# Kernel optimization log

Measured on AMD Instinct MI355X. Metric: run time of the kernel, lower is better.

## Reference

```python
import jax, jax.numpy as jnp
import numpy as np

B, S, D, H = 2, 2048, 1024, 16
HD = D // H  # head_dim = 64


def setup_inputs() -> dict:
    key = jax.random.key(0)
    ks = jax.random.split(key, 11)
    sc = 0.02
    inp = {
        "q": jax.random.normal(ks[0], (B, S, D), jnp.float32),
        "k": jax.random.normal(ks[1], (B, S, D), jnp.float32),
        "v": jax.random.normal(ks[2], (B, S, D), jnp.float32),
        # causal mask, broadcast over batch and heads; mask==0 positions get -1e9
        "mask": jnp.tril(jnp.ones((S, S), dtype=bool))[None, None, :, :],
        "Wq": jax.random.normal(ks[3], (D, D), jnp.float32) * sc,
        "bq": jnp.zeros((D,), jnp.float32),
        "Wk": jax.random.normal(ks[4], (D, D), jnp.float32) * sc,
        "bk": jnp.zeros((D,), jnp.float32),
        "Wv": jax.random.normal(ks[5], (D, D), jnp.float32) * sc,
        "bv": jnp.zeros((D,), jnp.float32),
        "Wo": jax.random.normal(ks[6], (D, D), jnp.float32) * sc,
        "bo": jnp.zeros((D,), jnp.float32),
    }
    return inp


def reference(q, k, v, Wq, bq, Wk, bk, Wv, bv, Wo, bo, mask):
    b, s, d = q.shape
    scale = 1.0 / jnp.sqrt(jnp.asarray(HD, q.dtype))

    def proj(x, W, bias):
        # nn.Linear: x @ W.T + b ; then split heads -> [b, h, s, hd]
        return (x @ W.T + bias).reshape(b, -1, H, HD).transpose(0, 2, 1, 3)

    Qh = proj(q, Wq, bq)
    Kh = proj(k, Wk, bk)
    Vh = proj(v, Wv, bv)

    scores = jnp.einsum("bhqd,bhkd->bhqk", Qh, Kh) * scale
    scores = jnp.where(mask, scores, jnp.asarray(-1e9, scores.dtype))
    probs = jax.nn.softmax(scores, axis=-1)
    attn = jnp.einsum("bhqk,bhkd->bhqd", probs, Vh)
    attn = attn.transpose(0, 2, 1, 3).reshape(b, -1, d)
    return attn @ Wo.T + bo
```

## Files before the change

### kernel.cpp

```cpp
#include <hip/hip_runtime.h>
#include <math.h>

#define B_ 2
#define S_ 2048
#define D_ 1024
#define H_ 16
#define HD_ 64

typedef __bf16 bf16;
typedef bf16 bf16x8_t __attribute__((ext_vector_type(8)));
typedef short s16x8 __attribute__((ext_vector_type(8)));
typedef float f32x4 __attribute__((ext_vector_type(4)));

static __device__ __forceinline__ f32x4 mfma16(s16x8 a, s16x8 b, f32x4 c) {
  return __builtin_amdgcn_mfma_f32_16x16x32_bf16(a, b, c, 0, 0, 0);
}

static __device__ __forceinline__ s16x8 cvt2x4(f32x4 a, f32x4 b) {
  bf16x8_t t;
  t[0] = (bf16)a[0]; t[1] = (bf16)a[1]; t[2] = (bf16)a[2]; t[3] = (bf16)a[3];
  t[4] = (bf16)b[0]; t[5] = (bf16)b[1]; t[6] = (bf16)b[2]; t[7] = (bf16)b[3];
  return __builtin_bit_cast(s16x8, t);
}

static __device__ __forceinline__ void gl16(const bf16* g, bf16* l) {
  __builtin_amdgcn_global_load_lds((const __attribute__((address_space(1))) void*)g,
                                   (__attribute__((address_space(3))) void*)l, 16, 0, 0);
}

__global__ __launch_bounds__(256) void cvt_w(
    const float* __restrict__ Wq, const float* __restrict__ Wk,
    const float* __restrict__ Wv, bf16* __restrict__ dst) {
  const float* s = blockIdx.y == 0 ? Wq : (blockIdx.y == 1 ? Wk : Wv);
  bf16* d = dst + (size_t)blockIdx.y * D_ * D_;
  const int i = (blockIdx.x * 256 + threadIdx.x) * 8;
  f32x4 a = *(const f32x4*)(s + i);
  f32x4 b = *(const f32x4*)(s + i + 4);
  *(s16x8*)(d + i) = cvt2x4(a, b);
}

__global__ __launch_bounds__(256) void cvt_w1(
    const float* __restrict__ W, bf16* __restrict__ dst) {
  const int i = (blockIdx.x * 256 + threadIdx.x) * 8;
  f32x4 a = *(const f32x4*)(W + i);
  f32x4 b = *(const f32x4*)(W + i + 4);
  *(s16x8*)(dst + i) = cvt2x4(a, b);
}

__global__ __launch_bounds__(256) void qkv_gemm(
    const float* __restrict__ q, const float* __restrict__ k, const float* __restrict__ v,
    const bf16* __restrict__ Wb,
    const float* __restrict__ bq, const float* __restrict__ bk, const float* __restrict__ bv,
    bf16* __restrict__ Qh, bf16* __restrict__ Kh, bf16* __restrict__ Vt) {
  __shared__ bf16 lA[128][72];
  __shared__ bf16 lB[128][64];
  const int tid = threadIdx.x, lane = tid & 63, wave = tid >> 6;
  const int wsel = blockIdx.y >> 3;
  const int col0 = (blockIdx.y & 7) * 128;
  const int row0 = blockIdx.x * 128;
  const float* X = wsel == 0 ? q : (wsel == 1 ? k : v);
  const bf16* W = Wb + (size_t)wsel * D_ * D_;
  const float* bias = wsel == 0 ? bq : (wsel == 1 ? bk : bv);

  const int lr = lane & 15, g = lane >> 4, lk = g * 8;
  const int wrow = (wave >> 1) * 64, wcol = (wave & 1) * 64;

  const int arow = tid >> 1, aseg = (tid & 1) * 32;
  const float* Xp = X + (size_t)(row0 + arow) * D_ + aseg;

  const bf16* Wp = W + (size_t)(col0 + wave * 32 + (lane >> 3)) * D_ +
                   (size_t)(((lane & 7) ^ ((lane >> 3) & 7)) * 8);
  bf16* lBw = &lB[wave * 32][0];

  f32x4 acc[4][4] = {};
  f32x4 xr[8];
#pragma unroll
  for (int j = 0; j < 8; j++) xr[j] = *(const f32x4*)(Xp + j * 4);

  for (int kk = 0; kk < D_; kk += 64) {
    __syncthreads();
#pragma unroll
    for (int p = 0; p < 4; p++)
      *(s16x8*)&lA[arow][aseg + p * 8] = cvt2x4(xr[2 * p], xr[2 * p + 1]);
#pragma unroll
    for (int i = 0; i < 4; i++)
      gl16(Wp + (size_t)i * 8 * D_ + kk, lBw + i * 8 * 64);
    __syncthreads();
    if (kk + 64 < D_) {
#pragma unroll
      for (int j = 0; j < 8; j++) xr[j] = *(const f32x4*)(Xp + kk + 64 + j * 4);
    }

    s16x8 af[4][2], bfr[4][2];
#pragma unroll
    for (int mi = 0; mi < 4; mi++)
#pragma unroll
      for (int kd = 0; kd < 2; kd++)
        af[mi][kd] = *(const s16x8*)&lA[wrow + mi * 16 + lr][kd * 32 + lk];
#pragma unroll
    for (int ni = 0; ni < 4; ni++)
#pragma unroll
      for (int kd = 0; kd < 2; kd++)
        bfr[ni][kd] = *(const s16x8*)((const bf16*)lB +
                        (size_t)(wcol + ni * 16 + lr) * 64 +
                        (((4 * kd + g) ^ (lr & 7)) * 8));
    __builtin_amdgcn_s_setprio(1);
#pragma unroll
    for (int mi = 0; mi < 4; mi++)
#pragma unroll
      for (int ni = 0; ni < 4; ni++)
#pragma unroll
        for (int kd = 0; kd < 2; kd++)
          acc[mi][ni] = mfma16(af[mi][kd], bfr[ni][kd], acc[mi][ni]);
    __builtin_amdgcn_s_setprio(0);
  }

  const int rb = g * 4;
#pragma unroll
  for (int mi = 0; mi < 4; mi++) {
#pragma unroll
    for (int ni = 0; ni < 4; ni++) {
      const int col = col0 + wcol + ni * 16 + lr;
      const int h = col >> 6, hd = col & 63;
      const float bvv = bias[col];
#pragma unroll
      for (int r = 0; r < 4; r++) {
        const int row = row0 + wrow + mi * 16 + rb + r;
        const int b = row >> 11, s = row & (S_ - 1);
        const float val = acc[mi][ni][r] + bvv;
        if (wsel == 0)
          Qh[(((size_t)(b * H_ + h)) * S_ + s) * HD_ + hd] = (bf16)(val * 0.125f);
        else if (wsel == 1)
          Kh[(((size_t)(b * H_ + h)) * S_ + s) * HD_ + hd] = (bf16)val;
        else
          Vt[(((size_t)(b * H_ + h)) * HD_ + hd) * S_ + s] = (bf16)val;
      }
    }
  }
}

__global__ __launch_bounds__(256) void out_gemm(
    const bf16* __restrict__ X, const bf16* __restrict__ W,
    const float* __restrict__ bias, float* __restrict__ Y) {
  __shared__ bf16 lA[64][64];
  __shared__ bf16 lB[128][64];
  const int tid = threadIdx.x, lane = tid & 63, wave = tid >> 6;
  const int row0 = blockIdx.x * 64, col0 = blockIdx.y * 128;
  const int lr = lane & 15, g = lane >> 4, lk = g * 8;
  const int wrow = (wave >> 1) * 32, wcol = (wave & 1) * 64;
  const int csw = ((lane & 7) ^ ((lane >> 3) & 7)) * 8;

  const bf16* Ap = X + (size_t)(row0 + wave * 16 + (lane >> 3)) * D_ + csw;
  const bf16* Wp = W + (size_t)(col0 + wave * 32 + (lane >> 3)) * D_ + csw;
  bf16* lAw = &lA[wave * 16][0];
  bf16* lBw = &lB[wave * 32][0];

  f32x4 acc[2][4] = {};
  for (int kk = 0; kk < D_; kk += 64) {
    __syncthreads();
#pragma unroll
    for (int i = 0; i < 2; i++) gl16(Ap + (size_t)i * 8 * D_ + kk, lAw + i * 8 * 64);
#pragma unroll
    for (int i = 0; i < 4; i++) gl16(Wp + (size_t)i * 8 * D_ + kk, lBw + i * 8 * 64);
    __syncthreads();

    s16x8 af[2][2], bfr[4][2];
#pragma unroll
    for (int mi = 0; mi < 2; mi++)
#pragma unroll
      for (int kd = 0; kd < 2; kd++)
        af[mi][kd] = *(const s16x8*)((const bf16*)lA +
                       (size_t)(wrow + mi * 16 + lr) * 64 +
                       (((4 * kd + g) ^ (lr & 7)) * 8));
#pragma unroll
    for (int ni = 0; ni < 4; ni++)
#pragma unroll
      for (int kd = 0; kd < 2; kd++)
        bfr[ni][kd] = *(const s16x8*)((const bf16*)lB +
                        (size_t)(wcol + ni * 16 + lr) * 64 +
                        (((4 * kd + g) ^ (lr & 7)) * 8));
    __builtin_amdgcn_s_setprio(1);
#pragma unroll
    for (int mi = 0; mi < 2; mi++)
#pragma unroll
      for (int ni = 0; ni < 4; ni++)
#pragma unroll
        for (int kd = 0; kd < 2; kd++)
          acc[mi][ni] = mfma16(af[mi][kd], bfr[ni][kd], acc[mi][ni]);
    __builtin_amdgcn_s_setprio(0);
  }

  const int rb = g * 4;
#pragma unroll
  for (int mi = 0; mi < 2; mi++) {
#pragma unroll
    for (int ni = 0; ni < 4; ni++) {
      const int col = col0 + wcol + ni * 16 + lr;
      const float bvv = bias[col];
#pragma unroll
      for (int r = 0; r < 4; r++) {
        const int row = row0 + wrow + mi * 16 + rb + r;
        Y[(size_t)row * D_ + col] = acc[mi][ni][r] + bvv;
      }
    }
  }
}

__global__ __launch_bounds__(256) void attn_fwd(
    const bf16* __restrict__ Qh, const bf16* __restrict__ Kh,
    const bf16* __restrict__ Vt, bf16* __restrict__ attnO) {
  __shared__ bf16 k_lds[64][72];
  __shared__ bf16 vt_lds[64][72];
  __shared__ bf16 p_lds[4][32][72];
  __shared__ float red_lds[4][32];

  const int tid = threadIdx.x;
  const int lane = tid & 63, wave = tid >> 6;
  const int lr = lane & 15, g = lane >> 4, lk = g * 8, rb = g * 4;

  const int bidx = blockIdx.x;
  const int qb = 15 - (bidx >> 5);
  const int bh = bidx & 31;
  const int bb = bh >> 4, hh = bh & 15;
  const int q0w = qb * 128 + wave * 32;

  const bf16* Q = Qh + (size_t)bh * S_ * HD_;
  const bf16* K = Kh + (size_t)bh * S_ * HD_;
  const bf16* Vp = Vt + (size_t)bh * HD_ * S_;

  s16x8 qf[2][2];
#pragma unroll
  for (int qfi = 0; qfi < 2; qfi++)
#pragma unroll
    for (int kd = 0; kd < 2; kd++)
      qf[qfi][kd] = *(const s16x8*)(Q + (size_t)(q0w + qfi * 16 + lr) * HD_ + kd * 32 + lk);

  f32x4 o[2][4] = {};
  float m_run[2] = {-INFINITY, -INFINITY};
  float l_run[2] = {0.0f, 0.0f};

  const int srow = tid >> 2, d0 = (tid & 3) << 4;
  const int ntiles = qb * 2 + 2;

  s16x8 kr0, kr1, vr0, vr1;
  {
    const bf16* kp = K + (size_t)srow * HD_ + d0;
    kr0 = *(const s16x8*)kp;
    kr1 = *(const s16x8*)(kp + 8);
    const bf16* vp = Vp + (size_t)srow * S_ + d0;
    vr0 = *(const s16x8*)vp;
    vr1 = *(const s16x8*)(vp + 8);
  }

  for (int t = 0; t < ntiles; t++) {
    const int k0 = t * 64;
    __syncthreads();
    *(s16x8*)&k_lds[srow][d0] = kr0;
    *(s16x8*)&k_lds[srow][d0 + 8] = kr1;
    *(s16x8*)&vt_lds[srow][d0] = vr0;
    *(s16x8*)&vt_lds[srow][d0 + 8] = vr1;
    __syncthreads();
    if (t + 1 < ntiles) {
      const int kn = k0 + 64;
      const bf16* kp = K + (size_t)(kn + srow) * HD_ + d0;
      kr0 = *(const s16x8*)kp;
      kr1 = *(const s16x8*)(kp + 8);
      const bf16* vp = Vp + (size_t)srow * S_ + kn + d0;
      vr0 = *(const s16x8*)vp;
      vr1 = *(const s16x8*)(vp + 8);
    }

    if (k0 <= q0w + 31) {
      const bool doMask = (k0 + 63 > q0w);
      s16x8 kfr[4][2];
#pragma unroll
      for (int kf = 0; kf < 4; kf++)
#pragma unroll
        for (int kd = 0; kd < 2; kd++)
          kfr[kf][kd] = *(const s16x8*)&k_lds[kf * 16 + lr][kd * 32 + lk];
      f32x4 s[4][2];
#pragma unroll
      for (int kf = 0; kf < 4; kf++)
#pragma unroll
        for (int qfi = 0; qfi < 2; qfi++) s[kf][qfi] = (f32x4){0.f, 0.f, 0.f, 0.f};
      __builtin_amdgcn_s_setprio(1);
#pragma unroll
      for (int kf = 0; kf < 4; kf++)
#pragma unroll
        for (int qfi = 0; qfi < 2; qfi++)
#pragma unroll
          for (int kd = 0; kd < 2; kd++)
            s[kf][qfi] = mfma16(kfr[kf][kd], qf[qfi][kd], s[kf][qfi]);
      __builtin_amdgcn_s_setprio(0);

#pragma unroll
      for (int qfi = 0; qfi < 2; qfi++) {
        const int qg = q0w + qfi * 16 + lr;
        if (doMask) {
#pragma unroll
          for (int kf = 0; kf < 4; kf++)
#pragma unroll
            for (int r = 0; r < 4; r++)
              if (k0 + kf * 16 + rb + r > qg) s[kf][qfi][r] = -INFINITY;
        }
        float mx = fmaxf(fmaxf(s[0][qfi][0], s[0][qfi][1]), fmaxf(s[0][qfi][2], s[0][qfi][3]));
#pragma unroll
        for (int kf = 1; kf < 4; kf++)
          mx = fmaxf(mx, fmaxf(fmaxf(s[kf][qfi][0], s[kf][qfi][1]),
                               fmaxf(s[kf][qfi][2], s[kf][qfi][3])));
        mx = fmaxf(mx, __shfl_xor(mx, 16));
        mx = fmaxf(mx, __shfl_xor(mx, 32));
        const float mo = m_run[qfi];
        const float mn = fmaxf(mo, mx);
        const float corr = exp2f((mo - mn) * 1.44269504f);
        float ps = 0.0f;
#pragma unroll
        for (int kf = 0; kf < 4; kf++)
#pragma unroll
          for (int r = 0; r < 4; r++) {
            const float p = exp2f((s[kf][qfi][r] - mn) * 1.44269504f);
            s[kf][qfi][r] = p;
            ps += p;
          }
        ps += __shfl_xor(ps, 16);
        ps += __shfl_xor(ps, 32);
        l_run[qfi] = l_run[qfi] * corr + ps;
        m_run[qfi] = mn;
        if (g == 0) red_lds[wave][qfi * 16 + lr] = corr;
#pragma unroll
        for (int kf = 0; kf < 4; kf++)
#pragma unroll
          for (int rp = 0; rp < 2; rp++) {
            unsigned int lo = (unsigned int)__builtin_bit_cast(
                unsigned short, (bf16)s[kf][qfi][2 * rp]);
            unsigned int hi = (unsigned int)__builtin_bit_cast(
                unsigned short, (bf16)s[kf][qfi][2 * rp + 1]);
            *(unsigned int*)&p_lds[wave][qfi * 16 + lr][kf * 16 + rb + 2 * rp] =
                lo | (hi << 16);
          }
      }
#pragma unroll
      for (int rf = 0; rf < 2; rf++) {
        f32x4 c4 = *(const f32x4*)&red_lds[wave][rf * 16 + rb];
#pragma unroll
        for (int df = 0; df < 4; df++)
#pragma unroll
          for (int r = 0; r < 4; r++) o[rf][df][r] *= c4[r];
      }
      s16x8 vfr[4][2];
#pragma unroll
      for (int df = 0; df < 4; df++)
#pragma unroll
        for (int kk = 0; kk < 2; kk++)
          vfr[df][kk] = *(const s16x8*)&vt_lds[df * 16 + lr][kk * 32 + lk];
      __builtin_amdgcn_s_setprio(1);
#pragma unroll
      for (int rf = 0; rf < 2; rf++) {
        s16x8 pa[2];
#pragma unroll
        for (int kk = 0; kk < 2; kk++)
          pa[kk] = *(const s16x8*)&p_lds[wave][rf * 16 + lr][kk * 32 + lk];
#pragma unroll
        for (int df = 0; df < 4; df++)
#pragma unroll
          for (int kk = 0; kk < 2; kk++)
            o[rf][df] = mfma16(pa[kk], vfr[df][kk], o[rf][df]);
      }
      __builtin_amdgcn_s_setprio(0);
    }
  }

  if (g == 0) {
    red_lds[wave][lr] = l_run[0];
    red_lds[wave][16 + lr] = l_run[1];
  }
#pragma unroll
  for (int rf = 0; rf < 2; rf++) {
    f32x4 l4 = *(const f32x4*)&red_lds[wave][rf * 16 + rb];
    float inv[4];
#pragma unroll
    for (int r = 0; r < 4; r++) inv[r] = 1.0f / l4[r];
#pragma unroll
    for (int df = 0; df < 4; df++)
#pragma unroll
      for (int r = 0; r < 4; r++) {
        const int srw = q0w + rf * 16 + rb + r;
        const int dcol = df * 16 + lr;
        attnO[((size_t)(bb * S_ + srw)) * D_ + hh * HD_ + dcol] =
            (bf16)(o[rf][df][r] * inv[r]);
      }
  }
}

extern "C" void kernel_launch(void* const* d_in, const int* in_sizes, int n_in,
                              void* d_out, int out_size, void* d_ws, size_t ws_size,
                              hipStream_t stream) {
  const float* q  = (const float*)d_in[0];
  const float* k  = (const float*)d_in[1];
  const float* v  = (const float*)d_in[2];
  const float* Wq = (const float*)d_in[4];
  const float* bq = (const float*)d_in[5];
  const float* Wk = (const float*)d_in[6];
  const float* bk = (const float*)d_in[7];
  const float* Wv = (const float*)d_in[8];
  const float* bv = (const float*)d_in[9];
  const float* Wo = (const float*)d_in[10];
  const float* bo = (const float*)d_in[11];
  float* out = (float*)d_out;

  const size_t NE = (size_t)B_ * S_ * D_;
  bf16* Qh    = (bf16*)d_ws;
  bf16* Kh    = Qh + NE;
  bf16* Vt    = Kh + NE;
  bf16* WbQKV = Vt + NE;
  bf16* attnB = Vt + NE;
  bf16* WoB   = (bf16*)d_ws;

  cvt_w<<<dim3(512, 3), 256, 0, stream>>>(Wq, Wk, Wv, WbQKV);
  qkv_gemm<<<dim3(32, 24), 256, 0, stream>>>(q, k, v, WbQKV, bq, bk, bv, Qh, Kh, Vt);
  attn_fwd<<<512, 256, 0, stream>>>(Qh, Kh, Vt, attnB);
  cvt_w1<<<512, 256, 0, stream>>>(Wo, WoB);
  out_gemm<<<dim3(64, 8), 256, 0, stream>>>(attnB, WoB, bo, out);
}
```

Baseline: 288.9 us.

## Double-buffer LDS tiles in QKV and output projection GEMMs

Both projection GEMMs now keep two LDS buffers for the A and W tiles. Each iteration issues the next tile's global-to-LDS loads before the MFMAs on the current tile, and one combined waitcnt plus barrier at the end of the iteration replaces the two __syncthreads per iteration. The goal is to hide global load latency behind compute. The cost is twice the LDS per block, which can lower occupancy, and the fence waits on all outstanding loads, which may limit how much overlap is gained.

After: 292.2 us. Within noise of the previous version (+1.1%).

```diff
diff --git a/kernel.cpp b/kernel.cpp
--- a/kernel.cpp
+++ b/kernel.cpp
@@ -26,6 +26,12 @@
 static __device__ __forceinline__ void gl16(const bf16* g, bf16* l) {
   __builtin_amdgcn_global_load_lds((const __attribute__((address_space(1))) void*)g,
                                    (__attribute__((address_space(3))) void*)l, 16, 0, 0);
+}
+
+static __device__ __forceinline__ void fence_barrier() {
+  asm volatile("s_waitcnt vmcnt(0) lgkmcnt(0)" ::: "memory");
+  __builtin_amdgcn_s_barrier();
+  asm volatile("" ::: "memory");
 }
 
 __global__ __launch_bounds__(256) void cvt_w(
@@ -52,8 +58,8 @@
     const bf16* __restrict__ Wb,
     const float* __restrict__ bq, const float* __restrict__ bk, const float* __restrict__ bv,
     bf16* __restrict__ Qh, bf16* __restrict__ Kh, bf16* __restrict__ Vt) {
-  __shared__ bf16 lA[128][72];
-  __shared__ bf16 lB[128][64];
+  __shared__ bf16 lA[2][128][72];
+  __shared__ bf16 lB[2][128][64];
   const int tid = threadIdx.x, lane = tid & 63, wave = tid >> 6;
   const int wsel = blockIdx.y >> 3;
   const int col0 = (blockIdx.y & 7) * 128;
@@ -70,25 +76,35 @@
 
   const bf16* Wp = W + (size_t)(col0 + wave * 32 + (lane >> 3)) * D_ +
                    (size_t)(((lane & 7) ^ ((lane >> 3) & 7)) * 8);
-  bf16* lBw = &lB[wave * 32][0];
 
   f32x4 acc[4][4] = {};
   f32x4 xr[8];
+
 #pragma unroll
   for (int j = 0; j < 8; j++) xr[j] = *(const f32x4*)(Xp + j * 4);
-
-  for (int kk = 0; kk < D_; kk += 64) {
-    __syncthreads();
-#pragma unroll
-    for (int p = 0; p < 4; p++)
-      *(s16x8*)&lA[arow][aseg + p * 8] = cvt2x4(xr[2 * p], xr[2 * p + 1]);
-#pragma unroll
-    for (int i = 0; i < 4; i++)
-      gl16(Wp + (size_t)i * 8 * D_ + kk, lBw + i * 8 * 64);
-    __syncthreads();
-    if (kk + 64 < D_) {
-#pragma unroll
-      for (int j = 0; j < 8; j++) xr[j] = *(const f32x4*)(Xp + kk + 64 + j * 4);
+#pragma unroll
+  for (int i = 0; i < 4; i++) gl16(Wp + (size_t)i * 8 * D_, &lB[0][wave * 32][0] + i * 8 * 64);
+#pragma unroll
+  for (int p = 0; p < 4; p++)
+    *(s16x8*)&lA[0][arow][aseg + p * 8] = cvt2x4(xr[2 * p], xr[2 * p + 1]);
+#pragma unroll
+  for (int j = 0; j < 8; j++) xr[j] = *(const f32x4*)(Xp + 64 + j * 4);
+  fence_barrier();
+
+  const int NT = D_ / 64;
+  for (int t = 0; t < NT; t++) {
+    const int cur = t & 1;
+    if (t + 1 < NT) {
+#pragma unroll
+      for (int i = 0; i < 4; i++)
+        gl16(Wp + (size_t)i * 8 * D_ + (t + 1) * 64, &lB[cur ^ 1][wave * 32][0] + i * 8 * 64);
+#pragma unroll
+      for (int p = 0; p < 4; p++)
+        *(s16x8*)&lA[cur ^ 1][arow][aseg + p * 8] = cvt2x4(xr[2 * p], xr[2 * p + 1]);
+      if (t + 2 < NT) {
+#pragma unroll
+        for (int j = 0; j < 8; j++) xr[j] = *(const f32x4*)(Xp + (t + 2) * 64 + j * 4);
+      }
     }
 
     s16x8 af[4][2], bfr[4][2];
@@ -96,12 +112,12 @@
     for (int mi = 0; mi < 4; mi++)
 #pragma unroll
       for (int kd = 0; kd < 2; kd++)
-        af[mi][kd] = *(const s16x8*)&lA[wrow + mi * 16 + lr][kd * 32 + lk];
+        af[mi][kd] = *(const s16x8*)&lA[cur][wrow + mi * 16 + lr][kd * 32 + lk];
 #pragma unroll
     for (int ni = 0; ni < 4; ni++)
 #pragma unroll
       for (int kd = 0; kd < 2; kd++)
-        bfr[ni][kd] = *(const s16x8*)((const bf16*)lB +
+        bfr[ni][kd] = *(const s16x8*)((const bf16*)lB + (size_t)cur * 128 * 64 +
                         (size_t)(wcol + ni * 16 + lr) * 64 +
                         (((4 * kd + g) ^ (lr & 7)) * 8));
     __builtin_amdgcn_s_setprio(1);
@@ -113,6 +129,7 @@
         for (int kd = 0; kd < 2; kd++)
           acc[mi][ni] = mfma16(af[mi][kd], bfr[ni][kd], acc[mi][ni]);
     __builtin_amdgcn_s_setprio(0);
+    if (t + 1 < NT) fence_barrier();
   }
 
   const int rb = g * 4;
@@ -142,8 +159,8 @@
 __global__ __launch_bounds__(256) void out_gemm(
     const bf16* __restrict__ X, const bf16* __restrict__ W,
     const float* __restrict__ bias, float* __restrict__ Y) {
-  __shared__ bf16 lA[64][64];
-  __shared__ bf16 lB[128][64];
+  __shared__ bf16 lA[2][64][64];
+  __shared__ bf16 lB[2][128][64];
   const int tid = threadIdx.x, lane = tid & 63, wave = tid >> 6;
   const int row0 = blockIdx.x * 64, col0 = blockIdx.y * 128;
   const int lr = lane & 15, g = lane >> 4, lk = g * 8;
@@ -152,31 +169,41 @@
 
   const bf16* Ap = X + (size_t)(row0 + wave * 16 + (lane >> 3)) * D_ + csw;
   const bf16* Wp = W + (size_t)(col0 + wave * 32 + (lane >> 3)) * D_ + csw;
-  bf16* lAw = &lA[wave * 16][0];
-  bf16* lBw = &lB[wave * 32][0];
 
   f32x4 acc[2][4] = {};
-  for (int kk = 0; kk < D_; kk += 64) {
-    __syncthreads();
-#pragma unroll
-    for (int i = 0; i < 2; i++) gl16(Ap + (size_t)i * 8 * D_ + kk, lAw + i * 8 * 64);
-#pragma unroll
-    for (int i = 0; i < 4; i++) gl16(Wp + (size_t)i * 8 * D_ + kk, lBw + i * 8 * 64);
-    __syncthreads();
+
+#pragma unroll
+  for (int i = 0; i < 2; i++) gl16(Ap + (size_t)i * 8 * D_, &lA[0][wave * 16][0] + i * 8 * 64);
+#pragma unroll
+  for (int i = 0; i < 4; i++) gl16(Wp + (size_t)i * 8 * D_, &lB[0][wave * 32][0] + i * 8 * 64);
+  fence_barrier();
+
+  const int NT = D_ / 64;
+  for (int t = 0; t < NT; t++) {
+    const int cur = t & 1;
+    if (t + 1 < NT) {
+      const int kk = (t + 1) * 64;
+#pragma unroll
+      for (int i = 0; i < 2; i++)
+        gl16(Ap + (size_t)i * 8 * D_ + kk, &lA[cur ^ 1][wave * 16][0] + i * 8 * 64);
+#pragma unroll
+      for (int i = 0; i < 4; i++)
+        gl16(Wp + (size_t)i * 8 * D_ + kk, &lB[cur ^ 1][wave * 32][0] + i * 8 * 64);
+    }
 
     s16x8 af[2][2], bfr[4][2];
 #pragma unroll
     for (int mi = 0; mi < 2; mi++)
 #pragma unroll
       for (int kd = 0; kd < 2; kd++)
-        af[mi][kd] = *(const s16x8*)((const bf16*)lA +
+        af[mi][kd] = *(const s16x8*)((const bf16*)lA + (size_t)cur * 64 * 64 +
                        (size_t)(wrow + mi * 16 + lr) * 64 +
                        (((4 * kd + g) ^ (lr & 7)) * 8));
 #pragma unroll
     for (int ni = 0; ni < 4; ni++)
 #pragma unroll
       for (int kd = 0; kd < 2; kd++)
-        bfr[ni][kd] = *(const s16x8*)((const bf16*)lB +
+        bfr[ni][kd] = *(const s16x8*)((const bf16*)lB + (size_t)cur * 128 * 64 +
                         (size_t)(wcol + ni * 16 + lr) * 64 +
                         (((4 * kd + g) ^ (lr & 7)) * 8));
     __builtin_amdgcn_s_setprio(1);
@@ -188,6 +215,7 @@
         for (int kd = 0; kd < 2; kd++)
           acc[mi][ni] = mfma16(af[mi][kd], bfr[ni][kd], acc[mi][ni]);
     __builtin_amdgcn_s_setprio(0);
+    if (t + 1 < NT) fence_barrier();
   }
 
   const int rb = g * 4;
```

## Widen QKV and output GEMM tiles to 256 columns with 512-thread blocks

Applied to the files above, without the earlier changes.

Both projection GEMMs now use 8-wave, 512-thread blocks covering 256 output columns instead of 128, which halves the grid and lets each A tile staged in LDS be reused across twice as many columns. The k-loop is split per 32-wide kd slice so fewer fragment registers are live at once, and the s_setprio hints are removed. The larger tiles mean fewer blocks on the GPU (384 and 256), which may leave some CUs idle, and the launch bounds ask for higher occupancy, which puts pressure on registers.

Measured after the change: 272.5 us. -5.7%, faster.

```diff
diff --git a/kernel.cpp b/kernel.cpp
--- a/kernel.cpp
+++ b/kernel.cpp
@@ -47,25 +47,25 @@
   *(s16x8*)(dst + i) = cvt2x4(a, b);
 }
 
-__global__ __launch_bounds__(256) void qkv_gemm(
+__global__ __launch_bounds__(512, 4) void qkv_gemm(
     const float* __restrict__ q, const float* __restrict__ k, const float* __restrict__ v,
     const bf16* __restrict__ Wb,
     const float* __restrict__ bq, const float* __restrict__ bk, const float* __restrict__ bv,
     bf16* __restrict__ Qh, bf16* __restrict__ Kh, bf16* __restrict__ Vt) {
   __shared__ bf16 lA[128][72];
-  __shared__ bf16 lB[128][64];
+  __shared__ bf16 lB[256][64];
   const int tid = threadIdx.x, lane = tid & 63, wave = tid >> 6;
-  const int wsel = blockIdx.y >> 3;
-  const int col0 = (blockIdx.y & 7) * 128;
+  const int wsel = blockIdx.y >> 2;
+  const int col0 = (blockIdx.y & 3) * 256;
   const int row0 = blockIdx.x * 128;
   const float* X = wsel == 0 ? q : (wsel == 1 ? k : v);
   const bf16* W = Wb + (size_t)wsel * D_ * D_;
   const float* bias = wsel == 0 ? bq : (wsel == 1 ? bk : bv);
 
   const int lr = lane & 15, g = lane >> 4, lk = g * 8;
-  const int wrow = (wave >> 1) * 64, wcol = (wave & 1) * 64;
-
-  const int arow = tid >> 1, aseg = (tid & 1) * 32;
+  const int wrow = (wave >> 2) * 64, wcol = (wave & 3) * 64;
+
+  const int arow = tid >> 2, aseg = (tid & 3) * 16;
   const float* Xp = X + (size_t)(row0 + arow) * D_ + aseg;
 
   const bf16* Wp = W + (size_t)(col0 + wave * 32 + (lane >> 3)) * D_ +
@@ -73,46 +73,40 @@
   bf16* lBw = &lB[wave * 32][0];
 
   f32x4 acc[4][4] = {};
-  f32x4 xr[8];
-#pragma unroll
-  for (int j = 0; j < 8; j++) xr[j] = *(const f32x4*)(Xp + j * 4);
+  f32x4 xr[4];
+#pragma unroll
+  for (int j = 0; j < 4; j++) xr[j] = *(const f32x4*)(Xp + j * 4);
 
   for (int kk = 0; kk < D_; kk += 64) {
     __syncthreads();
-#pragma unroll
-    for (int p = 0; p < 4; p++)
-      *(s16x8*)&lA[arow][aseg + p * 8] = cvt2x4(xr[2 * p], xr[2 * p + 1]);
+    *(s16x8*)&lA[arow][aseg] = cvt2x4(xr[0], xr[1]);
+    *(s16x8*)&lA[arow][aseg + 8] = cvt2x4(xr[2], xr[3]);
 #pragma unroll
     for (int i = 0; i < 4; i++)
       gl16(Wp + (size_t)i * 8 * D_ + kk, lBw + i * 8 * 64);
     __syncthreads();
     if (kk + 64 < D_) {
 #pragma unroll
-      for (int j = 0; j < 8; j++) xr[j] = *(const f32x4*)(Xp + kk + 64 + j * 4);
-    }
-
-    s16x8 af[4][2], bfr[4][2];
-#pragma unroll
-    for (int mi = 0; mi < 4; mi++)
-#pragma unroll
-      for (int kd = 0; kd < 2; kd++)
-        af[mi][kd] = *(const s16x8*)&lA[wrow + mi * 16 + lr][kd * 32 + lk];
-#pragma unroll
-    for (int ni = 0; ni < 4; ni++)
-#pragma unroll
-      for (int kd = 0; kd < 2; kd++)
-        bfr[ni][kd] = *(const s16x8*)((const bf16*)lB +
-                        (size_t)(wcol + ni * 16 + lr) * 64 +
-                        (((4 * kd + g) ^ (lr & 7)) * 8));
-    __builtin_amdgcn_s_setprio(1);
-#pragma unroll
-    for (int mi = 0; mi < 4; mi++)
+      for (int j = 0; j < 4; j++) xr[j] = *(const f32x4*)(Xp + kk + 64 + j * 4);
+    }
+
+#pragma unroll
+    for (int kd = 0; kd < 2; kd++) {
+      s16x8 af[4], bfr[4];
+#pragma unroll
+      for (int mi = 0; mi < 4; mi++)
+        af[mi] = *(const s16x8*)&lA[wrow + mi * 16 + lr][kd * 32 + lk];
 #pragma unroll
       for (int ni = 0; ni < 4; ni++)
-#pragma unroll
-        for (int kd = 0; kd < 2; kd++)
-          acc[mi][ni] = mfma16(af[mi][kd], bfr[ni][kd], acc[mi][ni]);
-    __builtin_amdgcn_s_setprio(0);
+        bfr[ni] = *(const s16x8*)((const bf16*)lB +
+                    (size_t)(wcol + ni * 16 + lr) * 64 +
+                    (((4 * kd + g) ^ (lr & 7)) * 8));
+#pragma unroll
+      for (int mi = 0; mi < 4; mi++)
+#pragma unroll
+        for (int ni = 0; ni < 4; ni++)
+          acc[mi][ni] = mfma16(af[mi], bfr[ni], acc[mi][ni]);
+    }
   }
 
   const int rb = g * 4;
@@ -139,55 +133,50 @@
   }
 }
 
-__global__ __launch_bounds__(256) void out_gemm(
+__global__ __launch_bounds__(512, 4) void out_gemm(
     const bf16* __restrict__ X, const bf16* __restrict__ W,
     const float* __restrict__ bias, float* __restrict__ Y) {
   __shared__ bf16 lA[64][64];
-  __shared__ bf16 lB[128][64];
+  __shared__ bf16 lB[256][64];
   const int tid = threadIdx.x, lane = tid & 63, wave = tid >> 6;
-  const int row0 = blockIdx.x * 64, col0 = blockIdx.y * 128;
+  const int row0 = blockIdx.x * 64, col0 = blockIdx.y * 256;
   const int lr = lane & 15, g = lane >> 4, lk = g * 8;
-  const int wrow = (wave >> 1) * 32, wcol = (wave & 1) * 64;
+  const int wrow = (wave >> 2) * 32, wcol = (wave & 3) * 64;
   const int csw = ((lane & 7) ^ ((lane >> 3) & 7)) * 8;
 
-  const bf16* Ap = X + (size_t)(row0 + wave * 16 + (lane >> 3)) * D_ + csw;
+  const bf16* Ap = X + (size_t)(row0 + wave * 8 + (lane >> 3)) * D_ + csw;
   const bf16* Wp = W + (size_t)(col0 + wave * 32 + (lane >> 3)) * D_ + csw;
-  bf16* lAw = &lA[wave * 16][0];
+  bf16* lAw = &lA[wave * 8][0];
   bf16* lBw = &lB[wave * 32][0];
 
   f32x4 acc[2][4] = {};
   for (int kk = 0; kk < D_; kk += 64) {
     __syncthreads();
-#pragma unroll
-    for (int i = 0; i < 2; i++) gl16(Ap + (size_t)i * 8 * D_ + kk, lAw + i * 8 * 64);
-#pragma unroll
-    for (int i = 0; i < 4; i++) gl16(Wp + (size_t)i * 8 * D_ + kk, lBw + i * 8 * 64);
-    __syncthreads();
-
-    s16x8 af[2][2], bfr[4][2];
-#pragma unroll
-    for (int mi = 0; mi < 2; mi++)
-#pragma unroll
-      for (int kd = 0; kd < 2; kd++)
-        af[mi][kd] = *(const s16x8*)((const bf16*)lA +
-                       (size_t)(wrow + mi * 16 + lr) * 64 +
-                       (((4 * kd + g) ^ (lr & 7)) * 8));
-#pragma unroll
-    for (int ni = 0; ni < 4; ni++)
-#pragma unroll
-      for (int kd = 0; kd < 2; kd++)
-        bfr[ni][kd] = *(const s16x8*)((const bf16*)lB +
-                        (size_t)(wcol + ni * 16 + lr) * 64 +
-                        (((4 * kd + g) ^ (lr & 7)) * 8));
-    __builtin_amdgcn_s_setprio(1);
-#pragma unroll
-    for (int mi = 0; mi < 2; mi++)
+    gl16(Ap + kk, lAw);
+#pragma unroll
+    for (int i = 0; i < 4; i++)
+      gl16(Wp + (size_t)i * 8 * D_ + kk, lBw + i * 8 * 64);
+    __syncthreads();
+
+#pragma unroll
+    for (int kd = 0; kd < 2; kd++) {
+      s16x8 af[2], bfr[4];
+#pragma unroll
+      for (int mi = 0; mi < 2; mi++)
+        af[mi] = *(const s16x8*)((const bf16*)lA +
+                   (size_t)(wrow + mi * 16 + lr) * 64 +
+                   (((4 * kd + g) ^ (lr & 7)) * 8));
 #pragma unroll
       for (int ni = 0; ni < 4; ni++)
-#pragma unroll
-        for (int kd = 0; kd < 2; kd++)
-          acc[mi][ni] = mfma16(af[mi][kd], bfr[ni][kd], acc[mi][ni]);
-    __builtin_amdgcn_s_setprio(0);
+        bfr[ni] = *(const s16x8*)((const bf16*)lB +
+                    (size_t)(wcol + ni * 16 + lr) * 64 +
+                    (((4 * kd + g) ^ (lr & 7)) * 8));
+#pragma unroll
+      for (int mi = 0; mi < 2; mi++)
+#pragma unroll
+        for (int ni = 0; ni < 4; ni++)
+          acc[mi][ni] = mfma16(af[mi], bfr[ni], acc[mi][ni]);
+    }
   }
 
   const int rb = g * 4;
@@ -417,8 +406,8 @@
   bf16* WoB   = (bf16*)d_ws;
 
   cvt_w<<<dim3(512, 3), 256, 0, stream>>>(Wq, Wk, Wv, WbQKV);
-  qkv_gemm<<<dim3(32, 24), 256, 0, stream>>>(q, k, v, WbQKV, bq, bk, bv, Qh, Kh, Vt);
+  qkv_gemm<<<dim3(32, 12), 512, 0, stream>>>(q, k, v, WbQKV, bq, bk, bv, Qh, Kh, Vt);
   attn_fwd<<<512, 256, 0, stream>>>(Qh, Kh, Vt, attnB);
   cvt_w1<<<512, 256, 0, stream>>>(Wo, WoB);
-  out_gemm<<<dim3(64, 8), 256, 0, stream>>>(attnB, WoB, bo, out);
-}
+  out_gemm<<<dim3(64, 4), 512, 0, stream>>>(attnB, WoB, bo, out);
+}
```
